# Kernel optimization log

Hardware: AMD Instinct MI355X
Metric: run time of the kernel (lower is better)

Reference implementation:

```python
import jax, jax.numpy as jnp
import numpy as np

NEG_SLOPE = 0.2  # PyG GATConv default negative_slope


def _gat_conv(x, edge_index, W, a_src, a_dst, b, concat):
    """One PyG-style GATConv layer (eval mode, add_self_loops=True).
    x: [N, F_in], W: [F_in, H*C], a_src/a_dst: [H, C], b: [H*C] or [C].
    """
    N = x.shape[0]
    H, C = a_src.shape
    loops = jnp.arange(N, dtype=edge_index.dtype)
    src = jnp.concatenate([edge_index[0], loops])  # [E+N]
    dst = jnp.concatenate([edge_index[1], loops])
    h = (x @ W).reshape(N, H, C)                   # [N,H,C]
    al_s = jnp.einsum('nhc,hc->nh', h, a_src)      # [N,H]
    al_d = jnp.einsum('nhc,hc->nh', h, a_dst)
    e = jax.nn.leaky_relu(al_s[src] + al_d[dst], NEG_SLOPE)  # [E+N, H]
    # segment softmax over incoming edges of each dst node
    m = jax.lax.stop_gradient(jax.ops.segment_max(e, dst, num_segments=N))
    ex = jnp.exp(e - m[dst])
    denom = jax.ops.segment_sum(ex, dst, num_segments=N)
    alpha = ex / denom[dst]                        # [E+N, H]
    out = jax.ops.segment_sum(h[src] * alpha[:, :, None], dst, num_segments=N)  # [N,H,C]
    out = out.reshape(N, H * C) if concat else out.mean(axis=1)
    return out + b


def setup_inputs() -> dict:
    key = jax.random.key(0)
    ks = jax.random.split(key, 10)
    N, E, F_IN = 100000, 1600000, 128
    H1, C1 = 4, 32   # layer 1: concat -> 128
    H2, C2 = 1, 64   # layer 2: mean   -> 64
    x = jax.random.normal(ks[0], (N, F_IN), dtype=jnp.float32)
    edge_index = jax.random.randint(ks[1], (2, E), 0, N, dtype=jnp.int32)
    s = 0.1
    return {
        'x': x,
        'edge_index': edge_index,
        'W1': jax.random.normal(ks[2], (F_IN, H1 * C1), dtype=jnp.float32) * s,
        'a1_src': jax.random.normal(ks[3], (H1, C1), dtype=jnp.float32) * s,
        'a1_dst': jax.random.normal(ks[4], (H1, C1), dtype=jnp.float32) * s,
        'b1': jnp.zeros((H1 * C1,), dtype=jnp.float32),
        'W2': jax.random.normal(ks[5], (H1 * C1, H2 * C2), dtype=jnp.float32) * s,
        'a2_src': jax.random.normal(ks[6], (H2, C2), dtype=jnp.float32) * s,
        'a2_dst': jax.random.normal(ks[7], (H2, C2), dtype=jnp.float32) * s,
        'b2': jnp.zeros((C2,), dtype=jnp.float32),
    }


def reference(x, edge_index, W1, a1_src, a1_dst, b1, W2, a2_src, a2_dst, b2):
    h = _gat_conv(x, edge_index, W1, a1_src, a1_dst, b1, concat=True)   # [N,128]
    h = jax.nn.elu(h)                                                   # dropout is identity in eval
    out = _gat_conv(h, edge_index, W2, a2_src, a2_dst, b2, concat=False)  # [N,64]
    return out
```

## Files before the change

kernel.cpp:

```cpp
#include <hip/hip_runtime.h>
#include <hip/hip_bf16.h>
#include <math.h>

static constexpr float NEG_SLOPE = 0.2f;
static constexpr float NEG_BIG = -3.0e38f;

typedef __attribute__((ext_vector_type(8))) short short8;
typedef __attribute__((ext_vector_type(4))) float f32x4;

__device__ __forceinline__ float blo(unsigned u) { return __uint_as_float(u << 16); }
__device__ __forceinline__ float bhi(unsigned u) { return __uint_as_float(u & 0xffff0000u); }
__device__ __forceinline__ unsigned pack2(float a, float b) {
  __hip_bfloat162 t = __float22bfloat162_rn(make_float2(a, b));
  union { __hip_bfloat162 b; unsigned u; } v;
  v.b = t;
  return v.u;
}

__global__ void k_prep_w(const float* __restrict__ W, uint4* __restrict__ out, int BN) {
  const int i = blockIdx.x * blockDim.x + threadIdx.x;
  if (i >= BN * 16) return;
  const int col = i >> 4;
  const int chunk = (i & 15) ^ (col & 7);
  const float* wp = W + (size_t)chunk * 8 * BN + col;
  uint4 u;
  u.x = pack2(wp[0 * BN], wp[1 * BN]);
  u.y = pack2(wp[2 * BN], wp[3 * BN]);
  u.z = pack2(wp[4 * BN], wp[5 * BN]);
  u.w = pack2(wp[6 * BN], wp[7 * BN]);
  out[i] = u;
}

template <int BN, int HEADS>
__global__ __launch_bounds__(256) void k_mfma_gemm(
    const float* __restrict__ x, const uint4* __restrict__ wsw,
    const float* __restrict__ a_src, const float* __restrict__ a_dst,
    __hip_bfloat16* __restrict__ h_out, float* __restrict__ als,
    float* __restrict__ ald, int N) {
  constexpr int NTILES = BN / 16;
  __shared__ unsigned char Xl[128 * 256];
  __shared__ unsigned char Wl[BN * 256];
  const int tid = threadIdx.x;
  const int lane = tid & 63;
  const int wid = tid >> 6;
  const int base = blockIdx.x * 128;

  {
    uint4* dst = (uint4*)Wl;
    for (int i = tid; i < BN * 16; i += 256) dst[i] = wsw[i];
  }
  for (int it = 0; it < 8; ++it) {
    const int i = it * 256 + tid;
    const int r = i >> 4, c = i & 15;
    const int g = base + r;
    float4 f0 = make_float4(0.f, 0.f, 0.f, 0.f), f1 = f0;
    if (g < N) {
      const float* xp = x + (size_t)g * 128 + c * 8;
      f0 = *(const float4*)xp;
      f1 = *(const float4*)(xp + 4);
    }
    uint4 u;
    u.x = pack2(f0.x, f0.y);
    u.y = pack2(f0.z, f0.w);
    u.z = pack2(f1.x, f1.y);
    u.w = pack2(f1.z, f1.w);
    *(uint4*)(Xl + r * 256 + ((c * 16) ^ ((r & 7) << 4))) = u;
  }
  __syncthreads();

  const int lg = lane >> 4;
  const int ll = lane & 15;

  union U { uint4 u; short8 s; };
  short8 afr[2][4];
#pragma unroll
  for (int rt = 0; rt < 2; ++rt) {
    const int row = wid * 32 + rt * 16 + ll;
    const unsigned char* rp = Xl + row * 256;
    const int swz = (row & 7) << 4;
#pragma unroll
    for (int ks = 0; ks < 4; ++ks) {
      U t;
      t.u = *(const uint4*)(rp + ((ks * 64 + lg * 16) ^ swz));
      afr[rt][ks] = t.s;
    }
  }

  f32x4 acc[2][NTILES];
#pragma unroll
  for (int rt = 0; rt < 2; ++rt)
#pragma unroll
    for (int t = 0; t < NTILES; ++t) acc[rt][t] = (f32x4){0.f, 0.f, 0.f, 0.f};

#pragma unroll
  for (int t = 0; t < NTILES; ++t) {
    const int col = t * 16 + ll;
    const unsigned char* cp = Wl + col * 256;
    const int swz = (col & 7) << 4;
#pragma unroll
    for (int ks = 0; ks < 4; ++ks) {
      U b;
      b.u = *(const uint4*)(cp + ((ks * 64 + lg * 16) ^ swz));
      acc[0][t] = __builtin_amdgcn_mfma_f32_16x16x32_bf16(afr[0][ks], b.s, acc[0][t], 0, 0, 0);
      acc[1][t] = __builtin_amdgcn_mfma_f32_16x16x32_bf16(afr[1][ks], b.s, acc[1][t], 0, 0, 0);
    }
  }

  float asv[NTILES], adv[NTILES];
#pragma unroll
  for (int t = 0; t < NTILES; ++t) {
    asv[t] = a_src[t * 16 + ll];
    adv[t] = a_dst[t * 16 + ll];
  }
#pragma unroll
  for (int rt = 0; rt < 2; ++rt) {
#pragma unroll
    for (int r = 0; r < 4; ++r) {
      const int row = base + wid * 32 + rt * 16 + lg * 4 + r;
      if (HEADS == 4) {
        float ps[4], pd[4];
#pragma unroll
        for (int h = 0; h < 4; ++h) {
          ps[h] = acc[rt][2 * h][r] * asv[2 * h] + acc[rt][2 * h + 1][r] * asv[2 * h + 1];
          pd[h] = acc[rt][2 * h][r] * adv[2 * h] + acc[rt][2 * h + 1][r] * adv[2 * h + 1];
#pragma unroll
          for (int off = 1; off < 16; off <<= 1) {
            ps[h] += __shfl_xor(ps[h], off, 64);
            pd[h] += __shfl_xor(pd[h], off, 64);
          }
        }
        if (ll == 0 && row < N) {
          ((float4*)als)[row] = make_float4(ps[0], ps[1], ps[2], ps[3]);
          ((float4*)ald)[row] = make_float4(pd[0], pd[1], pd[2], pd[3]);
        }
      } else {
        float ps = 0.f, pd = 0.f;
#pragma unroll
        for (int t = 0; t < NTILES; ++t) {
          ps = fmaf(acc[rt][t][r], asv[t], ps);
          pd = fmaf(acc[rt][t][r], adv[t], pd);
        }
#pragma unroll
        for (int off = 1; off < 16; off <<= 1) {
          ps += __shfl_xor(ps, off, 64);
          pd += __shfl_xor(pd, off, 64);
        }
        if (ll == 0 && row < N) {
          als[row] = ps;
          ald[row] = pd;
        }
      }
    }
  }

  __syncthreads();
#pragma unroll
  for (int rt = 0; rt < 2; ++rt) {
#pragma unroll
    for (int t = 0; t < NTILES; ++t) {
#pragma unroll
      for (int r = 0; r < 4; ++r) {
        const float v = acc[rt][t][r];
        const float vn = __shfl_xor(v, 1, 64);
        if (!(lane & 1)) {
          const int row = wid * 32 + rt * 16 + lg * 4 + r;
          *(unsigned*)(Xl + row * (BN * 2) + (t * 16 + ll) * 2) = pack2(v, vn);
        }
      }
    }
  }
  __syncthreads();
  {
    constexpr int U4 = 128 * BN / 8;
    constexpr int U4R = BN / 8;
    for (int i = tid; i < U4; i += 256) {
      const int row = i / U4R;
      const int g = base + row;
      if (g < N)
        *(uint4*)((unsigned short*)h_out + (size_t)g * BN + (i % U4R) * 8) = ((uint4*)Xl)[i];
    }
  }
}

__global__ void k_fill1(int* __restrict__ cnt, int N) {
  int i = blockIdx.x * blockDim.x + threadIdx.x;
  if (i < N) cnt[i] = 1;
}

__global__ void k_count(const int* __restrict__ edst, int* __restrict__ cnt, int E) {
  int i = blockIdx.x * blockDim.x + threadIdx.x;
  if (i < E) atomicAdd(cnt + edst[i], 1);
}

__global__ void k_scan_local(const int* __restrict__ cnt, int* __restrict__ rowptr,
                             int* __restrict__ bsum, int N) {
  __shared__ int lds[256];
  const int tid = threadIdx.x;
  const int base = blockIdx.x * 1024;
  int vals[4], tsum = 0;
#pragma unroll
  for (int q = 0; q < 4; ++q) {
    int i = base + tid * 4 + q;
    vals[q] = (i < N) ? cnt[i] : 0;
    tsum += vals[q];
  }
  lds[tid] = tsum;
  __syncthreads();
  for (int off = 1; off < 256; off <<= 1) {
    int t = (tid >= off) ? lds[tid - off] : 0;
    __syncthreads();
    lds[tid] += t;
    __syncthreads();
  }
  int run = lds[tid] - tsum;
  if (tid == 255) bsum[blockIdx.x] = lds[255];
#pragma unroll
  for (int q = 0; q < 4; ++q) {
    int i = base + tid * 4 + q;
    if (i < N) rowptr[i] = run;
    run += vals[q];
  }
}

__global__ void k_scan_bsum(int* __restrict__ bsum, int nb) {
  __shared__ int lds[1024];
  const int tid = threadIdx.x;
  int v = (tid < nb) ? bsum[tid] : 0;
  lds[tid] = v;
  __syncthreads();
  for (int off = 1; off < 1024; off <<= 1) {
    int t = (tid >= off) ? lds[tid - off] : 0;
    __syncthreads();
    lds[tid] += t;
    __syncthreads();
  }
  bsum[tid] = lds[tid] - v;
}

__global__ void k_scan_add(const int* __restrict__ bsum, int* __restrict__ rowptr,
                           int* __restrict__ cursor, int N, int total) {
  int i = blockIdx.x * blockDim.x + threadIdx.x;
  if (i < N) {
    int r = rowptr[i] + bsum[i >> 10];
    rowptr[i] = r;
    cursor[i] = r;
  } else if (i == N) {
    rowptr[N] = total;
  }
}

__global__ void k_build_part(const int* __restrict__ esrc, const int* __restrict__ edst,
                             int* __restrict__ cursor, int* __restrict__ nbr, int E, int N) {
  constexpr int NPARTS = 16;
  const int xcd = blockIdx.x & 7;
  const int span = (N + NPARTS - 1) / NPARTS;
  const int gid = (int)(blockIdx.x >> 3) * blockDim.x + threadIdx.x;
  const int stride = (int)(gridDim.x >> 3) * blockDim.x;
  const int E4 = E >> 2;
#pragma unroll
  for (int s = 0; s < NPARTS / 8; ++s) {
    const int p = s * 8 + xcd;
    const int lo = p * span;
    const int hi = min(N, lo + span);
    for (int i = gid; i < E4; i += stride) {
      const int4 d4 = ((const int4*)edst)[i];
      if (d4.x >= lo && d4.x < hi) nbr[atomicAdd(cursor + d4.x, 1)] = esrc[i * 4 + 0];
      if (d4.y >= lo && d4.y < hi) nbr[atomicAdd(cursor + d4.y, 1)] = esrc[i * 4 + 1];
      if (d4.z >= lo && d4.z < hi) nbr[atomicAdd(cursor + d4.z, 1)] = esrc[i * 4 + 2];
      if (d4.w >= lo && d4.w < hi) nbr[atomicAdd(cursor + d4.w, 1)] = esrc[i * 4 + 3];
    }
    for (int i = E4 * 4 + gid; i < E + N; i += stride) {
      const int d = i < E ? edst[i] : i - E;
      if (d >= lo && d < hi) {
        const int sn = i < E ? esrc[i] : i - E;
        nbr[atomicAdd(cursor + d, 1)] = sn;
      }
    }
  }
}

__global__ void k_gather_l1(const int* __restrict__ rowptr, const int* __restrict__ nbr,
                            const float* __restrict__ als, const float* __restrict__ ald,
                            const __hip_bfloat16* __restrict__ hfeat,
                            const float* __restrict__ bias,
                            float* __restrict__ out, int N) {
  __shared__ float alds[4][256];
  __shared__ int snlds[4][64];
  const int lane = threadIdx.x & 63;
  const int wid = threadIdx.x >> 6;
  const int node = (int)((blockIdx.x * blockDim.x + threadIdx.x) >> 6);
  if (node >= N) return;
  const int start = rowptr[node], end = rowptr[node + 1];
  const int deg = end - start;
  const float4 aldd = ((const float4*)ald)[node];

  float t[4];
  int myn = 0;
  {
    const int j = start + lane;
    if (j < end) {
      myn = nbr[j];
      const float4 av = ((const float4*)als)[myn];
      const float tr[4] = {av.x + aldd.x, av.y + aldd.y, av.z + aldd.z, av.w + aldd.w};
#pragma unroll
      for (int h = 0; h < 4; ++h) t[h] = tr[h] >= 0.f ? tr[h] : NEG_SLOPE * tr[h];
    } else {
#pragma unroll
      for (int h = 0; h < 4; ++h) t[h] = NEG_BIG;
    }
  }
  snlds[wid][lane] = myn;

  float Mh[4], rden[4], myex[4];
  if (deg <= 64) {
#pragma unroll
    for (int h = 0; h < 4; ++h) {
      float M = t[h];
#pragma unroll
      for (int off = 1; off < 64; off <<= 1) M = fmaxf(M, __shfl_xor(M, off, 64));
      const float e = __expf(t[h] - M);
      float sum = e;
#pragma unroll
      for (int off = 1; off < 64; off <<= 1) sum += __shfl_xor(sum, off, 64);
      Mh[h] = M;
      rden[h] = 1.f / sum;
      myex[h] = e * rden[h];
    }
  } else {
    float m[4], s[4];
#pragma unroll
    for (int h = 0; h < 4; ++h) { m[h] = t[h]; s[h] = 1.f; }
    for (int base = start + 64; base < end; base += 64) {
      const int j = base + lane;
      if (j < end) {
        const int sn = nbr[j];
        const float4 av = ((const float4*)als)[sn];
        const float tr[4] = {av.x + aldd.x, av.y + aldd.y, av.z + aldd.z, av.w + aldd.w};
#pragma unroll
        for (int h = 0; h < 4; ++h) {
          const float tv = tr[h] >= 0.f ? tr[h] : NEG_SLOPE * tr[h];
          const float M = fmaxf(m[h], tv);
          s[h] = s[h] * __expf(m[h] - M) + __expf(tv - M);
          m[h] = M;
        }
      }
    }
#pragma unroll
    for (int h = 0; h < 4; ++h) {
      float M = m[h];
#pragma unroll
      for (int off = 1; off < 64; off <<= 1) M = fmaxf(M, __shfl_xor(M, off, 64));
      float e = s[h] * __expf(m[h] - M);
#pragma unroll
      for (int off = 1; off < 64; off <<= 1) e += __shfl_xor(e, off, 64);
      Mh[h] = M;
      rden[h] = 1.f / e;
      myex[h] = __expf(t[h] - M) * rden[h];
    }
  }
  ((float4*)&alds[wid][0])[lane] = make_float4(myex[0], myex[1], myex[2], myex[3]);

  const int sub = lane >> 4;
  const int q = lane & 15;
  const int head = q >> 2;
  float acc[8];
#pragma unroll
  for (int k = 0; k < 8; ++k) acc[k] = 0.f;

  const int nq = deg < 64 ? deg : 64;
  for (int j0 = 0; j0 < nq; j0 += 4) {
    const int j = j0 + sub;
    const int sn = snlds[wid][j];
    const float a = alds[wid][j * 4 + head];
    const uint4 v = *(const uint4*)((const unsigned short*)hfeat + (size_t)sn * 128 + q * 8);
    acc[0] = fmaf(blo(v.x), a, acc[0]);
    acc[1] = fmaf(bhi(v.x), a, acc[1]);
    acc[2] = fmaf(blo(v.y), a, acc[2]);
    acc[3] = fmaf(bhi(v.y), a, acc[3]);
    acc[4] = fmaf(blo(v.z), a, acc[4]);
    acc[5] = fmaf(bhi(v.z), a, acc[5]);
    acc[6] = fmaf(blo(v.w), a, acc[6]);
    acc[7] = fmaf(bhi(v.w), a, acc[7]);
  }
  if (deg > 64) {
    const float Mm = head == 0 ? Mh[0] : head == 1 ? Mh[1] : head == 2 ? Mh[2] : Mh[3];
    const float rd = head == 0 ? rden[0] : head == 1 ? rden[1] : head == 2 ? rden[2] : rden[3];
    const float ad_ = head == 0 ? aldd.x : head == 1 ? aldd.y : head == 2 ? aldd.z : aldd.w;
    for (int j0 = 64; j0 < deg; j0 += 4) {
      const int j = j0 + sub;
      float a = 0.f;
      int sn = 0;
      if (j < deg) {
        sn = nbr[start + j];
        const float4 av = ((const float4*)als)[sn];
        const float as_ = head == 0 ? av.x : head == 1 ? av.y : head == 2 ? av.z : av.w;
        float tv = as_ + ad_;
        tv = tv >= 0.f ? tv : NEG_SLOPE * tv;
        a = __expf(tv - Mm) * rd;
      }
      const uint4 v = *(const uint4*)((const unsigned short*)hfeat + (size_t)sn * 128 + q * 8);
      acc[0] = fmaf(blo(v.x), a, acc[0]);
      acc[1] = fmaf(bhi(v.x), a, acc[1]);
      acc[2] = fmaf(blo(v.y), a, acc[2]);
      acc[3] = fmaf(bhi(v.y), a, acc[3]);
      acc[4] = fmaf(blo(v.z), a, acc[4]);
      acc[5] = fmaf(bhi(v.z), a, acc[5]);
      acc[6] = fmaf(blo(v.w), a, acc[6]);
      acc[7] = fmaf(bhi(v.w), a, acc[7]);
    }
  }

#pragma unroll
  for (int k = 0; k < 8; ++k) {
    acc[k] += __shfl_xor(acc[k], 16, 64);
    acc[k] += __shfl_xor(acc[k], 32, 64);
  }
  if (lane < 16) {
    const float4 b0 = ((const float4*)bias)[lane * 2];
    const float4 b1 = ((const float4*)bias)[lane * 2 + 1];
    float r[8] = {acc[0] + b0.x, acc[1] + b0.y, acc[2] + b0.z, acc[3] + b0.w,
                  acc[4] + b1.x, acc[5] + b1.y, acc[6] + b1.z, acc[7] + b1.w};
#pragma unroll
    for (int k = 0; k < 8; ++k) r[k] = r[k] > 0.f ? r[k] : __expf(r[k]) - 1.f;
    float4* op = (float4*)(out + (size_t)node * 128 + lane * 8);
    op[0] = make_float4(r[0], r[1], r[2], r[3]);
    op[1] = make_float4(r[4], r[5], r[6], r[7]);
  }
}

__global__ void k_gather_l2(const int* __restrict__ rowptr, const int* __restrict__ nbr,
                            const float* __restrict__ als, const float* __restrict__ ald,
                            const __hip_bfloat16* __restrict__ hfeat,
                            const float* __restrict__ bias,
                            float* __restrict__ out, int N) {
  __shared__ float alds[4][64];
  __shared__ int snlds[4][64];
  const int lane = threadIdx.x & 63;
  const int wid = threadIdx.x >> 6;
  const int node = (int)((blockIdx.x * blockDim.x + threadIdx.x) >> 6);
  if (node >= N) return;
  const int start = rowptr[node], end = rowptr[node + 1];
  const int deg = end - start;
  const float ald0 = ald[node];

  float t = NEG_BIG;
  int myn = 0;
  {
    const int j = start + lane;
    if (j < end) {
      myn = nbr[j];
      float tv = als[myn] + ald0;
      t = tv >= 0.f ? tv : NEG_SLOPE * tv;
    }
  }
  snlds[wid][lane] = myn;

  float M, rden;
  if (deg <= 64) {
    M = t;
#pragma unroll
    for (int off = 1; off < 64; off <<= 1) M = fmaxf(M, __shfl_xor(M, off, 64));
    const float e = __expf(t - M);
    float sum = e;
#pragma unroll
    for (int off = 1; off < 64; off <<= 1) sum += __shfl_xor(sum, off, 64);
    rden = 1.f / sum;
    alds[wid][lane] = e * rden;
  } else {
    float m = t, s = 1.f;
    for (int base = start + 64; base < end; base += 64) {
      const int j = base + lane;
      if (j < end) {
        float tv = als[nbr[j]] + ald0;
        tv = tv >= 0.f ? tv : NEG_SLOPE * tv;
        const float Mn = fmaxf(m, tv);
        s = s * __expf(m - Mn) + __expf(tv - Mn);
        m = Mn;
      }
    }
    M = m;
#pragma unroll
    for (int off = 1; off < 64; off <<= 1) M = fmaxf(M, __shfl_xor(M, off, 64));
    float e = s * __expf(m - M);
#pragma unroll
    for (int off = 1; off < 64; off <<= 1) e += __shfl_xor(e, off, 64);
    rden = 1.f / e;
    alds[wid][lane] = __expf(t - M) * rden;
  }

  const int sub = lane >> 3;
  const int q = lane & 7;
  float acc[8];
#pragma unroll
  for (int k = 0; k < 8; ++k) acc[k] = 0.f;

  const int nq = deg < 64 ? deg : 64;
  for (int j0 = 0; j0 < nq; j0 += 8) {
    const int j = j0 + sub;
    const int sn = snlds[wid][j];
    const float a = alds[wid][j];
    const uint4 v = *(const uint4*)((const unsigned short*)hfeat + (size_t)sn * 64 + q * 8);
    acc[0] = fmaf(blo(v.x), a, acc[0]);
    acc[1] = fmaf(bhi(v.x), a, acc[1]);
    acc[2] = fmaf(blo(v.y), a, acc[2]);
    acc[3] = fmaf(bhi(v.y), a, acc[3]);
    acc[4] = fmaf(blo(v.z), a, acc[4]);
    acc[5] = fmaf(bhi(v.z), a, acc[5]);
    acc[6] = fmaf(blo(v.w), a, acc[6]);
    acc[7] = fmaf(bhi(v.w), a, acc[7]);
  }
  if (deg > 64) {
    for (int j0 = 64; j0 < deg; j0 += 8) {
      const int j = j0 + sub;
      float a = 0.f;
      int sn = 0;
      if (j < deg) {
        sn = nbr[start + j];
        float tv = als[sn] + ald0;
        tv = tv >= 0.f ? tv : NEG_SLOPE * tv;
        a = __expf(tv - M) * rden;
      }
      const uint4 v = *(const uint4*)((const unsigned short*)hfeat + (size_t)sn * 64 + q * 8);
      acc[0] = fmaf(blo(v.x), a, acc[0]);
      acc[1] = fmaf(bhi(v.x), a, acc[1]);
      acc[2] = fmaf(blo(v.y), a, acc[2]);
      acc[3] = fmaf(bhi(v.y), a, acc[3]);
      acc[4] = fmaf(blo(v.z), a, acc[4]);
      acc[5] = fmaf(bhi(v.z), a, acc[5]);
      acc[6] = fmaf(blo(v.w), a, acc[6]);
      acc[7] = fmaf(bhi(v.w), a, acc[7]);
    }
  }

#pragma unroll
  for (int k = 0; k < 8; ++k) {
    acc[k] += __shfl_xor(acc[k], 8, 64);
    acc[k] += __shfl_xor(acc[k], 16, 64);
    acc[k] += __shfl_xor(acc[k], 32, 64);
  }
  if (lane < 8) {
    const float4 b0 = ((const float4*)bias)[lane * 2];
    const float4 b1 = ((const float4*)bias)[lane * 2 + 1];
    float4* op = (float4*)(out + (size_t)node * 64 + lane * 8);
    op[0] = make_float4(acc[0] + b0.x, acc[1] + b0.y, acc[2] + b0.z, acc[3] + b0.w);
    op[1] = make_float4(acc[4] + b1.x, acc[5] + b1.y, acc[6] + b1.z, acc[7] + b1.w);
  }
}

extern "C" void kernel_launch(void* const* d_in, const int* in_sizes, int n_in,
                              void* d_out, int out_size, void* d_ws, size_t ws_size,
                              hipStream_t stream) {
  const float* x   = (const float*)d_in[0];
  const int*   ei  = (const int*)d_in[1];
  const float* W1  = (const float*)d_in[2];
  const float* a1s = (const float*)d_in[3];
  const float* a1d = (const float*)d_in[4];
  const float* b1  = (const float*)d_in[5];
  const float* W2  = (const float*)d_in[6];
  const float* a2s = (const float*)d_in[7];
  const float* a2d = (const float*)d_in[8];
  const float* b2  = (const float*)d_in[9];

  const int N = in_sizes[0] / 128;
  const int E = in_sizes[1] / 2;
  const int* esrc = ei;
  const int* edst = ei + E;

  float* ws   = (float*)d_ws;
  __hip_bfloat16* h = (__hip_bfloat16*)ws;
  float* out1 = ws   + (size_t)N * 128;
  float* als  = out1 + (size_t)N * 128;
  float* ald  = als  + (size_t)N * 4;
  int* cnt    = (int*)(ald + (size_t)N * 4);
  int* rowptr = cnt + N;
  int* cursor = rowptr + N + 1;
  int* bsum   = cursor + N;
  int* nbr    = bsum + 1024;
  size_t off = ((size_t)((nbr + E + N) - (int*)ws) + 3) & ~(size_t)3;
  uint4* wsw1 = (uint4*)((int*)ws + off);
  uint4* wsw2 = wsw1 + 128 * 16;

  float* outF = (float*)d_out;

  const int total = E + N;
  const int nb = (N + 1023) / 1024;

  k_prep_w<<<(128 * 16 + 255) / 256, 256, 0, stream>>>(W1, wsw1, 128);
  k_prep_w<<<(64 * 16 + 255) / 256, 256, 0, stream>>>(W2, wsw2, 64);
  k_fill1<<<(N + 255) / 256, 256, 0, stream>>>(cnt, N);
  k_count<<<(E + 255) / 256, 256, 0, stream>>>(edst, cnt, E);
  k_scan_local<<<nb, 256, 0, stream>>>(cnt, rowptr, bsum, N);
  k_scan_bsum<<<1, 1024, 0, stream>>>(bsum, nb);
  k_scan_add<<<(N + 256) / 256, 256, 0, stream>>>(bsum, rowptr, cursor, N, total);
  k_build_part<<<1280, 256, 0, stream>>>(esrc, edst, cursor, nbr, E, N);

  k_mfma_gemm<128, 4><<<(N + 127) / 128, 256, 0, stream>>>(
      x, wsw1, a1s, a1d, h, als, ald, N);
  k_gather_l1<<<(N + 3) / 4, 256, 0, stream>>>(rowptr, nbr, als, ald, h, b1, out1, N);

  k_mfma_gemm<64, 1><<<(N + 127) / 128, 256, 0, stream>>>(
      out1, wsw2, a2s, a2d, h, als, ald, N);
  k_gather_l2<<<(N + 3) / 4, 256, 0, stream>>>(rowptr, nbr, als, ald, h, b2, outF, N);
}
```

Before: 362.9 us.

## Fold attention projections into GEMM, pack two nodes per wave in gathers

Precomputes W·a_src and W·a_dst as extra GEMM columns so the attention logits come out of the MFMA tile instead of shuffle reductions, and shares one LDS buffer between X and W tiles. The gather kernels now process two nodes per 64-lane wave (32 lanes each), with neighbor byte offsets prestored in LDS. Degree counting uses a memset and adds the self-loop in the scan, and edge partitioning drops to 8 parts. Logits are now computed from bf16-rounded fused weights, which changes precision, and wave-level packing adds divergence for high-degree nodes.

```diff
diff --git a/kernel.cpp b/kernel.cpp
--- a/kernel.cpp
+++ b/kernel.cpp
@@ -17,38 +17,58 @@
   return v.u;
 }
 
-__global__ void k_prep_w(const float* __restrict__ W, uint4* __restrict__ out, int BN) {
+template <int BN, int HEADS>
+__global__ void k_prep_w(const float* __restrict__ W, const float* __restrict__ as_,
+                         const float* __restrict__ ad_, uint4* __restrict__ out) {
+  constexpr int XC = BN + 16;
+  constexpr int C = BN / HEADS;
   const int i = blockIdx.x * blockDim.x + threadIdx.x;
-  if (i >= BN * 16) return;
+  if (i >= XC * 16) return;
   const int col = i >> 4;
   const int chunk = (i & 15) ^ (col & 7);
-  const float* wp = W + (size_t)chunk * 8 * BN + col;
+  float v[8];
+  if (col < BN) {
+#pragma unroll
+    for (int t = 0; t < 8; ++t) v[t] = W[(size_t)(chunk * 8 + t) * BN + col];
+  } else {
+    const int j = col - BN;
+#pragma unroll
+    for (int t = 0; t < 8; ++t) v[t] = 0.f;
+    if (j < 2 * HEADS) {
+      const int hh = (HEADS == 4) ? (j & 3) : 0;
+      const bool is_src = (HEADS == 4) ? (j < 4) : (j == 0);
+      const float* av = (is_src ? as_ : ad_) + hh * C;
+      const float* wb = W + hh * C;
+#pragma unroll
+      for (int t = 0; t < 8; ++t) {
+        float s = 0.f;
+        for (int c = 0; c < C; ++c) s = fmaf(wb[(size_t)(chunk * 8 + t) * BN + c], av[c], s);
+        v[t] = s;
+      }
+    }
+  }
   uint4 u;
-  u.x = pack2(wp[0 * BN], wp[1 * BN]);
-  u.y = pack2(wp[2 * BN], wp[3 * BN]);
-  u.z = pack2(wp[4 * BN], wp[5 * BN]);
-  u.w = pack2(wp[6 * BN], wp[7 * BN]);
+  u.x = pack2(v[0], v[1]);
+  u.y = pack2(v[2], v[3]);
+  u.z = pack2(v[4], v[5]);
+  u.w = pack2(v[6], v[7]);
   out[i] = u;
 }
 
 template <int BN, int HEADS>
 __global__ __launch_bounds__(256) void k_mfma_gemm(
     const float* __restrict__ x, const uint4* __restrict__ wsw,
-    const float* __restrict__ a_src, const float* __restrict__ a_dst,
     __hip_bfloat16* __restrict__ h_out, float* __restrict__ als,
     float* __restrict__ ald, int N) {
+  constexpr int XC = BN + 16;
   constexpr int NTILES = BN / 16;
-  __shared__ unsigned char Xl[128 * 256];
-  __shared__ unsigned char Wl[BN * 256];
+  constexpr int BUFSZ = (XC * 256 > 128 * 256) ? XC * 256 : 128 * 256;
+  __shared__ unsigned char buf[BUFSZ];
   const int tid = threadIdx.x;
   const int lane = tid & 63;
   const int wid = tid >> 6;
   const int base = blockIdx.x * 128;
 
-  {
-    uint4* dst = (uint4*)Wl;
-    for (int i = tid; i < BN * 16; i += 256) dst[i] = wsw[i];
-  }
   for (int it = 0; it < 8; ++it) {
     const int i = it * 256 + tid;
     const int r = i >> 4, c = i & 15;
@@ -64,19 +84,18 @@
     u.y = pack2(f0.z, f0.w);
     u.z = pack2(f1.x, f1.y);
     u.w = pack2(f1.z, f1.w);
-    *(uint4*)(Xl + r * 256 + ((c * 16) ^ ((r & 7) << 4))) = u;
+    *(uint4*)(buf + r * 256 + ((c * 16) ^ ((r & 7) << 4))) = u;
   }
   __syncthreads();
 
   const int lg = lane >> 4;
   const int ll = lane & 15;
-
   union U { uint4 u; short8 s; };
   short8 afr[2][4];
 #pragma unroll
   for (int rt = 0; rt < 2; ++rt) {
     const int row = wid * 32 + rt * 16 + ll;
-    const unsigned char* rp = Xl + row * 256;
+    const unsigned char* rp = buf + row * 256;
     const int swz = (row & 7) << 4;
 #pragma unroll
     for (int ks = 0; ks < 4; ++ks) {
@@ -85,17 +104,24 @@
       afr[rt][ks] = t.s;
     }
   }
-
-  f32x4 acc[2][NTILES];
+  __syncthreads();
+
+  {
+    uint4* dst = (uint4*)buf;
+    for (int i = tid; i < XC * 16; i += 256) dst[i] = wsw[i];
+  }
+  __syncthreads();
+
+  f32x4 acc[2][NTILES + 1];
 #pragma unroll
   for (int rt = 0; rt < 2; ++rt)
 #pragma unroll
-    for (int t = 0; t < NTILES; ++t) acc[rt][t] = (f32x4){0.f, 0.f, 0.f, 0.f};
-
-#pragma unroll
-  for (int t = 0; t < NTILES; ++t) {
+    for (int t = 0; t <= NTILES; ++t) acc[rt][t] = (f32x4){0.f, 0.f, 0.f, 0.f};
+
+#pragma unroll
+  for (int t = 0; t <= NTILES; ++t) {
     const int col = t * 16 + ll;
-    const unsigned char* cp = Wl + col * 256;
+    const unsigned char* cp = buf + col * 256;
     const int swz = (col & 7) << 4;
 #pragma unroll
     for (int ks = 0; ks < 4; ++ks) {
@@ -106,48 +132,19 @@
     }
   }
 
-  float asv[NTILES], adv[NTILES];
-#pragma unroll
-  for (int t = 0; t < NTILES; ++t) {
-    asv[t] = a_src[t * 16 + ll];
-    adv[t] = a_dst[t * 16 + ll];
-  }
 #pragma unroll
   for (int rt = 0; rt < 2; ++rt) {
 #pragma unroll
     for (int r = 0; r < 4; ++r) {
       const int row = base + wid * 32 + rt * 16 + lg * 4 + r;
-      if (HEADS == 4) {
-        float ps[4], pd[4];
-#pragma unroll
-        for (int h = 0; h < 4; ++h) {
-          ps[h] = acc[rt][2 * h][r] * asv[2 * h] + acc[rt][2 * h + 1][r] * asv[2 * h + 1];
-          pd[h] = acc[rt][2 * h][r] * adv[2 * h] + acc[rt][2 * h + 1][r] * adv[2 * h + 1];
-#pragma unroll
-          for (int off = 1; off < 16; off <<= 1) {
-            ps[h] += __shfl_xor(ps[h], off, 64);
-            pd[h] += __shfl_xor(pd[h], off, 64);
-          }
-        }
-        if (ll == 0 && row < N) {
-          ((float4*)als)[row] = make_float4(ps[0], ps[1], ps[2], ps[3]);
-          ((float4*)ald)[row] = make_float4(pd[0], pd[1], pd[2], pd[3]);
-        }
-      } else {
-        float ps = 0.f, pd = 0.f;
-#pragma unroll
-        for (int t = 0; t < NTILES; ++t) {
-          ps = fmaf(acc[rt][t][r], asv[t], ps);
-          pd = fmaf(acc[rt][t][r], adv[t], pd);
-        }
-#pragma unroll
-        for (int off = 1; off < 16; off <<= 1) {
-          ps += __shfl_xor(ps, off, 64);
-          pd += __shfl_xor(pd, off, 64);
-        }
-        if (ll == 0 && row < N) {
-          als[row] = ps;
-          ald[row] = pd;
+      if (row < N) {
+        const float v = acc[rt][NTILES][r];
+        if (HEADS == 4) {
+          if (ll < 4) als[(size_t)row * 4 + ll] = v;
+          else if (ll < 8) ald[(size_t)row * 4 + (ll - 4)] = v;
+        } else {
+          if (ll == 0) als[row] = v;
+          else if (ll == 1) ald[row] = v;
         }
       }
     }
@@ -164,7 +161,7 @@
         const float vn = __shfl_xor(v, 1, 64);
         if (!(lane & 1)) {
           const int row = wid * 32 + rt * 16 + lg * 4 + r;
-          *(unsigned*)(Xl + row * (BN * 2) + (t * 16 + ll) * 2) = pack2(v, vn);
+          *(unsigned*)(buf + row * (BN * 2) + (t * 16 + ll) * 2) = pack2(v, vn);
         }
       }
     }
@@ -177,14 +174,9 @@
       const int row = i / U4R;
       const int g = base + row;
       if (g < N)
-        *(uint4*)((unsigned short*)h_out + (size_t)g * BN + (i % U4R) * 8) = ((uint4*)Xl)[i];
-    }
-  }
-}
-
-__global__ void k_fill1(int* __restrict__ cnt, int N) {
-  int i = blockIdx.x * blockDim.x + threadIdx.x;
-  if (i < N) cnt[i] = 1;
+        *(uint4*)((unsigned short*)h_out + (size_t)g * BN + (i % U4R) * 8) = ((uint4*)buf)[i];
+    }
+  }
 }
 
 __global__ void k_count(const int* __restrict__ edst, int* __restrict__ cnt, int E) {
@@ -201,7 +193,7 @@
 #pragma unroll
   for (int q = 0; q < 4; ++q) {
     int i = base + tid * 4 + q;
-    vals[q] = (i < N) ? cnt[i] : 0;
+    vals[q] = (i < N) ? cnt[i] + 1 : 0;
     tsum += vals[q];
   }
   lds[tid] = tsum;
@@ -251,30 +243,26 @@
 
 __global__ void k_build_part(const int* __restrict__ esrc, const int* __restrict__ edst,
                              int* __restrict__ cursor, int* __restrict__ nbr, int E, int N) {
-  constexpr int NPARTS = 16;
-  const int xcd = blockIdx.x & 7;
+  constexpr int NPARTS = 8;
+  const int p = blockIdx.x & 7;
   const int span = (N + NPARTS - 1) / NPARTS;
+  const int lo = p * span;
+  const int hi = min(N, lo + span);
   const int gid = (int)(blockIdx.x >> 3) * blockDim.x + threadIdx.x;
   const int stride = (int)(gridDim.x >> 3) * blockDim.x;
   const int E4 = E >> 2;
-#pragma unroll
-  for (int s = 0; s < NPARTS / 8; ++s) {
-    const int p = s * 8 + xcd;
-    const int lo = p * span;
-    const int hi = min(N, lo + span);
-    for (int i = gid; i < E4; i += stride) {
-      const int4 d4 = ((const int4*)edst)[i];
-      if (d4.x >= lo && d4.x < hi) nbr[atomicAdd(cursor + d4.x, 1)] = esrc[i * 4 + 0];
-      if (d4.y >= lo && d4.y < hi) nbr[atomicAdd(cursor + d4.y, 1)] = esrc[i * 4 + 1];
-      if (d4.z >= lo && d4.z < hi) nbr[atomicAdd(cursor + d4.z, 1)] = esrc[i * 4 + 2];
-      if (d4.w >= lo && d4.w < hi) nbr[atomicAdd(cursor + d4.w, 1)] = esrc[i * 4 + 3];
-    }
-    for (int i = E4 * 4 + gid; i < E + N; i += stride) {
-      const int d = i < E ? edst[i] : i - E;
-      if (d >= lo && d < hi) {
-        const int sn = i < E ? esrc[i] : i - E;
-        nbr[atomicAdd(cursor + d, 1)] = sn;
-      }
+  for (int i = gid; i < E4; i += stride) {
+    const int4 d4 = ((const int4*)edst)[i];
+    if (d4.x >= lo && d4.x < hi) nbr[atomicAdd(cursor + d4.x, 1)] = esrc[i * 4 + 0];
+    if (d4.y >= lo && d4.y < hi) nbr[atomicAdd(cursor + d4.y, 1)] = esrc[i * 4 + 1];
+    if (d4.z >= lo && d4.z < hi) nbr[atomicAdd(cursor + d4.z, 1)] = esrc[i * 4 + 2];
+    if (d4.w >= lo && d4.w < hi) nbr[atomicAdd(cursor + d4.w, 1)] = esrc[i * 4 + 3];
+  }
+  for (int i = E4 * 4 + gid; i < E + N; i += stride) {
+    const int d = i < E ? edst[i] : i - E;
+    if (d >= lo && d < hi) {
+      const int sn = i < E ? esrc[i] : i - E;
+      nbr[atomicAdd(cursor + d, 1)] = sn;
     }
   }
 }
@@ -284,20 +272,26 @@
                             const __hip_bfloat16* __restrict__ hfeat,
                             const float* __restrict__ bias,
                             float* __restrict__ out, int N) {
-  __shared__ float alds[4][256];
-  __shared__ int snlds[4][64];
+  __shared__ float atab[4][2][4][40];
+  __shared__ unsigned otab[4][2][32];
   const int lane = threadIdx.x & 63;
   const int wid = threadIdx.x >> 6;
-  const int node = (int)((blockIdx.x * blockDim.x + threadIdx.x) >> 6);
-  if (node >= N) return;
-  const int start = rowptr[node], end = rowptr[node + 1];
+  const int half = lane >> 5;
+  const int l32 = lane & 31;
+  const int node = (int)((blockIdx.x * blockDim.x + threadIdx.x) >> 6) * 2 + half;
+  const bool valid = node < N;
+  int start = 0, end = 0;
+  if (valid) {
+    start = rowptr[node];
+    end = rowptr[node + 1];
+  }
   const int deg = end - start;
-  const float4 aldd = ((const float4*)ald)[node];
+  const float4 aldd = valid ? ((const float4*)ald)[node] : make_float4(0.f, 0.f, 0.f, 0.f);
 
   float t[4];
   int myn = 0;
   {
-    const int j = start + lane;
+    const int j = start + l32;
     if (j < end) {
       myn = nbr[j];
       const float4 av = ((const float4*)als)[myn];
@@ -309,19 +303,19 @@
       for (int h = 0; h < 4; ++h) t[h] = NEG_BIG;
     }
   }
-  snlds[wid][lane] = myn;
+  otab[wid][half][l32] = (unsigned)myn << 8;
 
   float Mh[4], rden[4], myex[4];
-  if (deg <= 64) {
+  if (deg <= 32) {
 #pragma unroll
     for (int h = 0; h < 4; ++h) {
       float M = t[h];
 #pragma unroll
-      for (int off = 1; off < 64; off <<= 1) M = fmaxf(M, __shfl_xor(M, off, 64));
+      for (int off = 1; off < 32; off <<= 1) M = fmaxf(M, __shfl_xor(M, off, 64));
       const float e = __expf(t[h] - M);
       float sum = e;
 #pragma unroll
-      for (int off = 1; off < 64; off <<= 1) sum += __shfl_xor(sum, off, 64);
+      for (int off = 1; off < 32; off <<= 1) sum += __shfl_xor(sum, off, 64);
       Mh[h] = M;
       rden[h] = 1.f / sum;
       myex[h] = e * rden[h];
@@ -329,9 +323,12 @@
   } else {
     float m[4], s[4];
 #pragma unroll
-    for (int h = 0; h < 4; ++h) { m[h] = t[h]; s[h] = 1.f; }
-    for (int base = start + 64; base < end; base += 64) {
-      const int j = base + lane;
+    for (int h = 0; h < 4; ++h) {
+      m[h] = t[h];
+      s[h] = (t[h] > NEG_BIG) ? 1.f : 0.f;
+    }
+    for (int b = start + 32; b < end; b += 32) {
+      const int j = b + l32;
       if (j < end) {
         const int sn = nbr[j];
         const float4 av = ((const float4*)als)[sn];
@@ -349,30 +346,34 @@
     for (int h = 0; h < 4; ++h) {
       float M = m[h];
 #pragma unroll
-      for (int off = 1; off < 64; off <<= 1) M = fmaxf(M, __shfl_xor(M, off, 64));
+      for (int off = 1; off < 32; off <<= 1) M = fmaxf(M, __shfl_xor(M, off, 64));
       float e = s[h] * __expf(m[h] - M);
 #pragma unroll
-      for (int off = 1; off < 64; off <<= 1) e += __shfl_xor(e, off, 64);
+      for (int off = 1; off < 32; off <<= 1) e += __shfl_xor(e, off, 64);
       Mh[h] = M;
       rden[h] = 1.f / e;
       myex[h] = __expf(t[h] - M) * rden[h];
     }
   }
-  ((float4*)&alds[wid][0])[lane] = make_float4(myex[0], myex[1], myex[2], myex[3]);
-
-  const int sub = lane >> 4;
-  const int q = lane & 15;
+#pragma unroll
+  for (int h = 0; h < 4; ++h) atab[wid][half][h][l32] = myex[h];
+
+  const int sub = l32 >> 4;
+  const int q = l32 & 15;
   const int head = q >> 2;
+  const char* hq = (const char*)hfeat + q * 16;
   float acc[8];
 #pragma unroll
   for (int k = 0; k < 8; ++k) acc[k] = 0.f;
 
-  const int nq = deg < 64 ? deg : 64;
-  for (int j0 = 0; j0 < nq; j0 += 4) {
+  const int nq = deg < 32 ? deg : 32;
+  const float* ap = &atab[wid][half][head][0];
+  const unsigned* op = &otab[wid][half][0];
+#pragma unroll 2
+  for (int j0 = 0; j0 < nq; j0 += 2) {
     const int j = j0 + sub;
-    const int sn = snlds[wid][j];
-    const float a = alds[wid][j * 4 + head];
-    const uint4 v = *(const uint4*)((const unsigned short*)hfeat + (size_t)sn * 128 + q * 8);
+    const float a = ap[j];
+    const uint4 v = *(const uint4*)(hq + op[j]);
     acc[0] = fmaf(blo(v.x), a, acc[0]);
     acc[1] = fmaf(bhi(v.x), a, acc[1]);
     acc[2] = fmaf(blo(v.y), a, acc[2]);
@@ -382,11 +383,11 @@
     acc[6] = fmaf(blo(v.w), a, acc[6]);
     acc[7] = fmaf(bhi(v.w), a, acc[7]);
   }
-  if (deg > 64) {
+  if (deg > 32) {
     const float Mm = head == 0 ? Mh[0] : head == 1 ? Mh[1] : head == 2 ? Mh[2] : Mh[3];
     const float rd = head == 0 ? rden[0] : head == 1 ? rden[1] : head == 2 ? rden[2] : rden[3];
     const float ad_ = head == 0 ? aldd.x : head == 1 ? aldd.y : head == 2 ? aldd.z : aldd.w;
-    for (int j0 = 64; j0 < deg; j0 += 4) {
+    for (int j0 = 32; j0 < deg; j0 += 2) {
       const int j = j0 + sub;
       float a = 0.f;
       int sn = 0;
@@ -398,7 +399,7 @@
         tv = tv >= 0.f ? tv : NEG_SLOPE * tv;
         a = __expf(tv - Mm) * rd;
       }
-      const uint4 v = *(const uint4*)((const unsigned short*)hfeat + (size_t)sn * 128 + q * 8);
+      const uint4 v = *(const uint4*)(hq + (size_t)sn * 256);
       acc[0] = fmaf(blo(v.x), a, acc[0]);
       acc[1] = fmaf(bhi(v.x), a, acc[1]);
       acc[2] = fmaf(blo(v.y), a, acc[2]);
@@ -411,20 +412,17 @@
   }
 
 #pragma unroll
-  for (int k = 0; k < 8; ++k) {
-    acc[k] += __shfl_xor(acc[k], 16, 64);
-    acc[k] += __shfl_xor(acc[k], 32, 64);
-  }
-  if (lane < 16) {
-    const float4 b0 = ((const float4*)bias)[lane * 2];
-    const float4 b1 = ((const float4*)bias)[lane * 2 + 1];
+  for (int k = 0; k < 8; ++k) acc[k] += __shfl_xor(acc[k], 16, 64);
+  if (valid && sub == 0) {
+    const float4 b0 = ((const float4*)bias)[q * 2];
+    const float4 b1 = ((const float4*)bias)[q * 2 + 1];
     float r[8] = {acc[0] + b0.x, acc[1] + b0.y, acc[2] + b0.z, acc[3] + b0.w,
                   acc[4] + b1.x, acc[5] + b1.y, acc[6] + b1.z, acc[7] + b1.w};
 #pragma unroll
     for (int k = 0; k < 8; ++k) r[k] = r[k] > 0.f ? r[k] : __expf(r[k]) - 1.f;
-    float4* op = (float4*)(out + (size_t)node * 128 + lane * 8);
-    op[0] = make_float4(r[0], r[1], r[2], r[3]);
-    op[1] = make_float4(r[4], r[5], r[6], r[7]);
+    float4* opo = (float4*)(out + (size_t)node * 128 + q * 8);
+    opo[0] = make_float4(r[0], r[1], r[2], r[3]);
+    opo[1] = make_float4(r[4], r[5], r[6], r[7]);
   }
 }
 
@@ -433,43 +431,47 @@
                             const __hip_bfloat16* __restrict__ hfeat,
                             const float* __restrict__ bias,
                             float* __restrict__ out, int N) {
-  __shared__ float alds[4][64];
-  __shared__ int snlds[4][64];
+  __shared__ float2 atab[4][2][36];
   const int lane = threadIdx.x & 63;
   const int wid = threadIdx.x >> 6;
-  const int node = (int)((blockIdx.x * blockDim.x + threadIdx.x) >> 6);
-  if (node >= N) return;
-  const int start = rowptr[node], end = rowptr[node + 1];
+  const int half = lane >> 5;
+  const int l32 = lane & 31;
+  const int node = (int)((blockIdx.x * blockDim.x + threadIdx.x) >> 6) * 2 + half;
+  const bool valid = node < N;
+  int start = 0, end = 0;
+  if (valid) {
+    start = rowptr[node];
+    end = rowptr[node + 1];
+  }
   const int deg = end - start;
-  const float ald0 = ald[node];
+  const float ald0 = valid ? ald[node] : 0.f;
 
   float t = NEG_BIG;
   int myn = 0;
   {
-    const int j = start + lane;
+    const int j = start + l32;
     if (j < end) {
       myn = nbr[j];
       float tv = als[myn] + ald0;
       t = tv >= 0.f ? tv : NEG_SLOPE * tv;
     }
   }
-  snlds[wid][lane] = myn;
-
-  float M, rden;
-  if (deg <= 64) {
+
+  float M, rden, myal;
+  if (deg <= 32) {
     M = t;
 #pragma unroll
-    for (int off = 1; off < 64; off <<= 1) M = fmaxf(M, __shfl_xor(M, off, 64));
+    for (int off = 1; off < 32; off <<= 1) M = fmaxf(M, __shfl_xor(M, off, 64));
     const float e = __expf(t - M);
     float sum = e;
 #pragma unroll
-    for (int off = 1; off < 64; off <<= 1) sum += __shfl_xor(sum, off, 64);
+    for (int off = 1; off < 32; off <<= 1) sum += __shfl_xor(sum, off, 64);
     rden = 1.f / sum;
-    alds[wid][lane] = e * rden;
+    myal = e * rden;
   } else {
-    float m = t, s = 1.f;
-    for (int base = start + 64; base < end; base += 64) {
-      const int j = base + lane;
+    float m = t, s = (t > NEG_BIG) ? 1.f : 0.f;
+    for (int b = start + 32; b < end; b += 32) {
+      const int j = b + l32;
       if (j < end) {
         float tv = als[nbr[j]] + ald0;
         tv = tv >= 0.f ? tv : NEG_SLOPE * tv;
@@ -480,26 +482,30 @@
     }
     M = m;
 #pragma unroll
-    for (int off = 1; off < 64; off <<= 1) M = fmaxf(M, __shfl_xor(M, off, 64));
+    for (int off = 1; off < 32; off <<= 1) M = fmaxf(M, __shfl_xor(M, off, 64));
     float e = s * __expf(m - M);
 #pragma unroll
-    for (int off = 1; off < 64; off <<= 1) e += __shfl_xor(e, off, 64);
+    for (int off = 1; off < 32; off <<= 1) e += __shfl_xor(e, off, 64);
     rden = 1.f / e;
-    alds[wid][lane] = __expf(t - M) * rden;
-  }
-
-  const int sub = lane >> 3;
-  const int q = lane & 7;
+    myal = __expf(t - M) * rden;
+  }
+  atab[wid][half][l32 < 36 ? l32 : 35] = make_float2(myal, __int_as_float(myn << 7));
+
+  const int sub = l32 >> 3;
+  const int q = l32 & 7;
+  const char* hq = (const char*)hfeat + q * 16;
   float acc[8];
 #pragma unroll
   for (int k = 0; k < 8; ++k) acc[k] = 0.f;
 
-  const int nq = deg < 64 ? deg : 64;
-  for (int j0 = 0; j0 < nq; j0 += 8) {
+  const int nq = deg < 32 ? deg : 32;
+  const float2* ap = &atab[wid][half][0];
+#pragma unroll 2
+  for (int j0 = 0; j0 < nq; j0 += 4) {
     const int j = j0 + sub;
-    const int sn = snlds[wid][j];
-    const float a = alds[wid][j];
-    const uint4 v = *(const uint4*)((const unsigned short*)hfeat + (size_t)sn * 64 + q * 8);
+    const float2 ao = ap[j];
+    const uint4 v = *(const uint4*)(hq + (unsigned)__float_as_int(ao.y));
+    const float a = ao.x;
     acc[0] = fmaf(blo(v.x), a, acc[0]);
     acc[1] = fmaf(bhi(v.x), a, acc[1]);
     acc[2] = fmaf(blo(v.y), a, acc[2]);
@@ -509,8 +515,8 @@
     acc[6] = fmaf(blo(v.w), a, acc[6]);
     acc[7] = fmaf(bhi(v.w), a, acc[7]);
   }
-  if (deg > 64) {
-    for (int j0 = 64; j0 < deg; j0 += 8) {
+  if (deg > 32) {
+    for (int j0 = 32; j0 < deg; j0 += 4) {
       const int j = j0 + sub;
       float a = 0.f;
       int sn = 0;
@@ -520,7 +526,7 @@
         tv = tv >= 0.f ? tv : NEG_SLOPE * tv;
         a = __expf(tv - M) * rden;
       }
-      const uint4 v = *(const uint4*)((const unsigned short*)hfeat + (size_t)sn * 64 + q * 8);
+      const uint4 v = *(const uint4*)(hq + (size_t)sn * 128);
       acc[0] = fmaf(blo(v.x), a, acc[0]);
       acc[1] = fmaf(bhi(v.x), a, acc[1]);
       acc[2] = fmaf(blo(v.y), a, acc[2]);
@@ -536,14 +542,13 @@
   for (int k = 0; k < 8; ++k) {
     acc[k] += __shfl_xor(acc[k], 8, 64);
     acc[k] += __shfl_xor(acc[k], 16, 64);
-    acc[k] += __shfl_xor(acc[k], 32, 64);
-  }
-  if (lane < 8) {
-    const float4 b0 = ((const float4*)bias)[lane * 2];
-    const float4 b1 = ((const float4*)bias)[lane * 2 + 1];
-    float4* op = (float4*)(out + (size_t)node * 64 + lane * 8);
-    op[0] = make_float4(acc[0] + b0.x, acc[1] + b0.y, acc[2] + b0.z, acc[3] + b0.w);
-    op[1] = make_float4(acc[4] + b1.x, acc[5] + b1.y, acc[6] + b1.z, acc[7] + b1.w);
+  }
+  if (valid && sub == 0 && q < 8) {
+    const float4 b0 = ((const float4*)bias)[q * 2];
+    const float4 b1 = ((const float4*)bias)[q * 2 + 1];
+    float4* opo = (float4*)(out + (size_t)node * 64 + q * 8);
+    opo[0] = make_float4(acc[0] + b0.x, acc[1] + b0.y, acc[2] + b0.z, acc[3] + b0.w);
+    opo[1] = make_float4(acc[4] + b1.x, acc[5] + b1.y, acc[6] + b1.z, acc[7] + b1.w);
   }
 }
 
@@ -578,27 +583,25 @@
   int* nbr    = bsum + 1024;
   size_t off = ((size_t)((nbr + E + N) - (int*)ws) + 3) & ~(size_t)3;
   uint4* wsw1 = (uint4*)((int*)ws + off);
-  uint4* wsw2 = wsw1 + 128 * 16;
+  uint4* wsw2 = wsw1 + 144 * 16;
 
   float* outF = (float*)d_out;
 
   const int total = E + N;
   const int nb = (N + 1023) / 1024;
 
-  k_prep_w<<<(128 * 16 + 255) / 256, 256, 0, stream>>>(W1, wsw1, 128);
-  k_prep_w<<<(64 * 16 + 255) / 256, 256, 0, stream>>>(W2, wsw2, 64);
-  k_fill1<<<(N + 255) / 256, 256, 0, stream>>>(cnt, N);
+  k_prep_w<128, 4><<<(144 * 16 + 255) / 256, 256, 0, stream>>>(W1, a1s, a1d, wsw1);
+  k_prep_w<64, 1><<<(80 * 16 + 255) / 256, 256, 0, stream>>>(W2, a2s, a2d, wsw2);
+  hipMemsetAsync(cnt, 0, (size_t)N * 4, stream);
   k_count<<<(E + 255) / 256, 256, 0, stream>>>(edst, cnt, E);
   k_scan_local<<<nb, 256, 0, stream>>>(cnt, rowptr, bsum, N);
   k_scan_bsum<<<1, 1024, 0, stream>>>(bsum, nb);
   k_scan_add<<<(N + 256) / 256, 256, 0, stream>>>(bsum, rowptr, cursor, N, total);
   k_build_part<<<1280, 256, 0, stream>>>(esrc, edst, cursor, nbr, E, N);
 
-  k_mfma_gemm<128, 4><<<(N + 127) / 128, 256, 0, stream>>>(
-      x, wsw1, a1s, a1d, h, als, ald, N);
-  k_gather_l1<<<(N + 3) / 4, 256, 0, stream>>>(rowptr, nbr, als, ald, h, b1, out1, N);
-
-  k_mfma_gemm<64, 1><<<(N + 127) / 128, 256, 0, stream>>>(
-      out1, wsw2, a2s, a2d, h, als, ald, N);
-  k_gather_l2<<<(N + 3) / 4, 256, 0, stream>>>(rowptr, nbr, als, ald, h, b2, outF, N);
-}
+  k_mfma_gemm<128, 4><<<(N + 127) / 128, 256, 0, stream>>>(x, wsw1, h, als, ald, N);
+  k_gather_l1<<<(N + 7) / 8, 256, 0, stream>>>(rowptr, nbr, als, ald, h, b1, out1, N);
+
+  k_mfma_gemm<64, 1><<<(N + 127) / 128, 256, 0, stream>>>(out1, wsw2, h, als, ald, N);
+  k_gather_l2<<<(N + 7) / 8, 256, 0, stream>>>(rowptr, nbr, als, ald, h, b2, outF, N);
+}
```

Measured after the change: 329.4 us. 1.1x faster.
